# Kernel tuning notes

Hardware: AMD Instinct MI355X
Metric: run time of the kernel (lower is better)

Reference implementation:

```python
import jax, jax.numpy as jnp
import numpy as np

NUM_HEADS = 16
N_EMBD = 1024
HEAD_SIZE = N_EMBD // NUM_HEADS
BLOCK_SIZE = 2048
B, T = 4, 2048


def setup_inputs() -> dict:
    key = jax.random.key(0)
    ks = jax.random.split(key, 6)
    x = jax.random.normal(ks[0], (B, T, N_EMBD), dtype=jnp.float32)
    s = 1.0 / np.sqrt(N_EMBD)
    # per-head q/k/v projections (bias=False), stacked over heads: [H, D, hs]
    Wq = jax.random.uniform(ks[1], (NUM_HEADS, N_EMBD, HEAD_SIZE), minval=-s, maxval=s, dtype=jnp.float32)
    Wk = jax.random.uniform(ks[2], (NUM_HEADS, N_EMBD, HEAD_SIZE), minval=-s, maxval=s, dtype=jnp.float32)
    Wv = jax.random.uniform(ks[3], (NUM_HEADS, N_EMBD, HEAD_SIZE), minval=-s, maxval=s, dtype=jnp.float32)
    # output projection nn.Linear(n_embd, n_embd): weight [D, D] (out, in) + bias [D]
    Wo = jax.random.uniform(ks[4], (N_EMBD, N_EMBD), minval=-s, maxval=s, dtype=jnp.float32)
    bo = jax.random.uniform(ks[5], (N_EMBD,), minval=-s, maxval=s, dtype=jnp.float32)
    return {"x": x, "Wq": Wq, "Wk": Wk, "Wv": Wv, "Wo": Wo, "bo": bo}


def _mha(x, Wq, Wk, Wv, Wo, bo):
    # project all heads at once: [B,T,D] x [H,D,hs] -> [B,H,T,hs]
    q = jnp.einsum("btd,hds->bhts", x, Wq)
    k = jnp.einsum("btd,hds->bhts", x, Wk)
    v = jnp.einsum("btd,hds->bhts", x, Wv)
    scale = jnp.asarray(HEAD_SIZE, x.dtype) ** -0.5
    scores = jnp.einsum("bhqs,bhks->bhqk", q, k) * scale  # [B,H,T,T]
    T_ = x.shape[1]
    causal = jnp.tril(jnp.ones((T_, T_), dtype=bool))
    scores = jnp.where(causal[None, None], scores, jnp.asarray(-jnp.inf, x.dtype))
    att = jax.nn.softmax(scores, axis=-1)
    out = jnp.einsum("bhqk,bhks->bhqs", att, v)  # [B,H,T,hs]
    # concat heads along last dim: [B,T,H*hs]
    out = out.transpose(0, 2, 1, 3).reshape(x.shape[0], T_, N_EMBD)
    # output projection (dropout=0.0 -> identity)
    return out @ Wo.T + bo


def reference(x, Wq, Wk, Wv, Wo, bo):
    return _mha(x, Wq, Wk, Wv, Wo, bo)
```

## Files before the change

### kernel.cpp

```cpp
#include <hip/hip_runtime.h>
#include <hip/hip_bf16.h>
#include <stdint.h>

typedef __bf16 bf16;
typedef __attribute__((ext_vector_type(8))) __bf16 bf16x8;
typedef __attribute__((ext_vector_type(4))) float f32x4;

#define NH     16
#define DM     1024
#define HS     64
#define BATCH  4
#define SEQ    2048
#define N_XE   (BATCH * SEQ * DM)
#define N_WOE  (DM * DM)

__device__ __forceinline__ void async16(void* lds, const void* g) {
  __builtin_amdgcn_global_load_lds(
      (const uint32_t __attribute__((address_space(1)))*)g,
      (uint32_t __attribute__((address_space(3)))*)lds,
      16, 0, 0);
}

__device__ __forceinline__ f32x4 mfma16(bf16x8 a, bf16x8 b, f32x4 c) {
  return __builtin_amdgcn_mfma_f32_16x16x32_bf16(a, b, c, 0, 0, 0);
}

__global__ void detect_mode(const unsigned short* __restrict__ x, int* flag) {
  int lane = threadIdx.x & 63;
  unsigned short v = x[2 * lane];
  int e = (v >> 7) & 0xFF;
  int sane = (e >= 90 && e <= 160) ? 1 : 0;
  #pragma unroll
  for (int s = 1; s < 64; s <<= 1) sane += __shfl_xor(sane, s, 64);
  if (threadIdx.x == 0) *flag = (sane >= 48) ? 0 : 1;
}

__global__ __launch_bounds__(256)
void convert_in(const void* __restrict__ x, const void* __restrict__ Wo,
                bf16* __restrict__ xb, bf16* __restrict__ Wob,
                const int* __restrict__ flagp) {
  const int f32m = *flagp;
  size_t base = ((size_t)blockIdx.x * 256 + threadIdx.x) * 8;
  const void* src; bf16* dst; size_t off;
  if (base < (size_t)N_XE) { src = x;  dst = xb;  off = base; }
  else                     { src = Wo; dst = Wob; off = base - N_XE; }
  if (f32m) {
    const float* s = (const float*)src + off;
    float4 a = *(const float4*)s;
    float4 b = *(const float4*)(s + 4);
    bf16x8 o;
    o[0] = (bf16)a.x; o[1] = (bf16)a.y; o[2] = (bf16)a.z; o[3] = (bf16)a.w;
    o[4] = (bf16)b.x; o[5] = (bf16)b.y; o[6] = (bf16)b.z; o[7] = (bf16)b.w;
    *(bf16x8*)(dst + off) = o;
  } else {
    *(bf16x8*)(dst + off) = *(const bf16x8*)((const bf16*)src + off);
  }
}

__global__ __launch_bounds__(256)
void transpose_w(const void* __restrict__ Wq, const void* __restrict__ Wk,
                 const void* __restrict__ Wv, bf16* __restrict__ WT,
                 const int* __restrict__ flagp) {
  __shared__ bf16 Ts[64][72];
  const int f32m = *flagp;
  const void* W = (blockIdx.y == 0) ? Wq : (blockIdx.y == 1) ? Wk : Wv;
  bf16* dst = WT + (size_t)blockIdx.y * DM * DM;
  const int h  = blockIdx.x >> 4;
  const int d0 = (blockIdx.x & 15) * 64;
  const int tid = threadIdx.x;
  #pragma unroll
  for (int p = 0; p < 2; ++p) {
    int idx = p * 256 + tid;
    int dr = idx >> 3, c = idx & 7;
    size_t eoff = (size_t)(h * DM + d0 + dr) * HS + c * 8;
    bf16x8 v;
    if (f32m) {
      const float* s = (const float*)W + eoff;
      #pragma unroll
      for (int j = 0; j < 8; ++j) v[j] = (bf16)s[j];
    } else {
      v = *(const bf16x8*)((const bf16*)W + eoff);
    }
    #pragma unroll
    for (int j = 0; j < 8; ++j) Ts[c * 8 + j][dr] = v[j];
  }
  __syncthreads();
  #pragma unroll
  for (int p = 0; p < 2; ++p) {
    int idx = p * 256 + tid;
    int sr = idx >> 3, c = idx & 7;
    bf16x8 v = *(const bf16x8*)(&Ts[sr][c * 8]);
    *(bf16x8*)(dst + (size_t)(h * 64 + sr) * DM + d0 + c * 8) = v;
  }
}

template<typename EpiF>
__device__ __forceinline__ void gemm128_bt(const bf16* __restrict__ A,
                                           const bf16* __restrict__ BT,
                                           int m0, int n0, EpiF epi) {
  __shared__ bf16 As[2][128 * 32];
  __shared__ bf16 Bs[2][128 * 32];
  const int tid  = threadIdx.x;
  const int wave = tid >> 6, lane = tid & 63;
  const int wr = wave >> 1, wc = wave & 1;
  const int fr = lane & 15, fg = lane >> 4;
  const int srow = lane >> 2;
  const int scb  = (lane & 3) * 16;
  f32x4 acc[4][4] = {};

  auto STAGE = [&](int buf, int k0) {
    #pragma unroll
    for (int i = 0; i < 2; ++i) {
      int chunk = wave * 2 + i;
      int row = chunk * 16 + srow;
      async16((char*)&As[buf][0] + chunk * 1024,
              (const char*)(A + (size_t)(m0 + row) * DM + k0) + scb);
      async16((char*)&Bs[buf][0] + chunk * 1024,
              (const char*)(BT + (size_t)(n0 + row) * DM + k0) + scb);
    }
  };

  STAGE(0, 0);
  #pragma unroll 1
  for (int t = 0; t < 32; ++t) {
    const int buf = t & 1;
    if (t + 1 < 32) {
      STAGE(buf ^ 1, (t + 1) * 32);
      asm volatile("s_waitcnt vmcnt(4)" ::: "memory");
    } else {
      asm volatile("s_waitcnt vmcnt(0)" ::: "memory");
    }
    __builtin_amdgcn_s_barrier();
    bf16x8 af[4], bv[4];
    #pragma unroll
    for (int mi = 0; mi < 4; ++mi)
      af[mi] = *(const bf16x8*)(&As[buf][(wr * 64 + mi * 16 + fr) * 32 + fg * 8]);
    #pragma unroll
    for (int ni = 0; ni < 4; ++ni)
      bv[ni] = *(const bf16x8*)(&Bs[buf][(wc * 64 + ni * 16 + fr) * 32 + fg * 8]);
    #pragma unroll
    for (int mi = 0; mi < 4; ++mi)
      #pragma unroll
      for (int ni = 0; ni < 4; ++ni)
        acc[mi][ni] = mfma16(af[mi], bv[ni], acc[mi][ni]);
    __builtin_amdgcn_s_barrier();
  }
  #pragma unroll
  for (int mi = 0; mi < 4; ++mi)
    #pragma unroll
    for (int ni = 0; ni < 4; ++ni)
      #pragma unroll
      for (int r = 0; r < 4; ++r) {
        int m = m0 + wr * 64 + mi * 16 + fg * 4 + r;
        int n = n0 + wc * 64 + ni * 16 + fr;
        epi(m, n, acc[mi][ni][r]);
      }
}

__global__ __launch_bounds__(256, 4)
void qkv_gemm(const bf16* __restrict__ x, const bf16* __restrict__ WT,
              bf16* __restrict__ Qb, bf16* __restrict__ Kb, bf16* __restrict__ Vt) {
  const int bid = blockIdx.x;
  const int m0 = (bid & 63) * 128;
  const int nz = bid >> 6;
  const int z  = nz >> 3;
  const int n0 = (nz & 7) * 128;
  const bf16* BT = WT + (size_t)z * DM * DM;
  gemm128_bt(x, BT, m0, n0, [&](int m, int n, float v) {
    int b = m >> 11, t = m & 2047, h = n >> 6, s = n & 63;
    if (z == 0)
      Qb[((size_t)(b * NH + h) * SEQ + t) * HS + s] = (bf16)v;
    else if (z == 1)
      Kb[((size_t)(b * NH + h) * SEQ + t) * HS + s] = (bf16)v;
    else
      Vt[((size_t)(b * NH + h) * HS + s) * SEQ + t] = (bf16)v;
  });
}

__global__ __launch_bounds__(256, 4)
void out_gemm(const bf16* __restrict__ att, const bf16* __restrict__ Wob,
              const void* __restrict__ bo, void* __restrict__ out,
              const int* __restrict__ flagp) {
  const int f32m = *flagp;
  const int bid = blockIdx.x;
  const int m0 = (bid & 63) * 128;
  const int n0 = (bid >> 6) * 128;
  gemm128_bt(att, Wob, m0, n0, [&](int m, int n, float v) {
    float bv = f32m ? ((const float*)bo)[n] : (float)((const bf16*)bo)[n];
    float o = v + bv;
    if (f32m) ((float*)out)[(size_t)m * DM + n] = o;
    else      ((bf16*)out)[(size_t)m * DM + n] = (bf16)o;
  });
}

#define KVB  64
__global__ __launch_bounds__(256, 2)
void attn_kernel(const bf16* __restrict__ Qb, const bf16* __restrict__ Kb,
                 const bf16* __restrict__ Vt, bf16* __restrict__ att) {
  __shared__ bf16 Ks[2][64][64];
  __shared__ bf16 Vs[2][64][64];
  __shared__ bf16 Ps[4][2][16][64];
  const int wave = threadIdx.x >> 6, lane = threadIdx.x & 63;
  const int fr = lane & 15, fg = lane >> 4;
  const int pair = blockIdx.x;
  const int bh = blockIdx.y;
  const bf16* Qp = Qb + (size_t)bh * SEQ * HS;
  const bf16* Kp = Kb + (size_t)bh * SEQ * HS;
  const bf16* Vp = Vt + (size_t)bh * HS * SEQ;
  const int b = bh >> 4, h = bh & 15;

  const int srow8 = lane >> 3;
  const int schk  = (lane & 7) ^ srow8;

  #pragma unroll
  for (int seg = 0; seg < 2; ++seg) {
    const int qb = seg == 0 ? (15 - pair) : pair;
    const int q0 = qb * 128 + wave * 32;
    const int kv_hi = q0 + 32;
    const int nt = (qb + 1) * 2;

    bf16x8 qf[2][2];
    #pragma unroll
    for (int qt = 0; qt < 2; ++qt)
      #pragma unroll
      for (int hh = 0; hh < 2; ++hh)
        qf[qt][hh] = *(const bf16x8*)(Qp + (size_t)(q0 + qt * 16 + fr) * HS + hh * 32 + fg * 8);

    float rs[2][4] = {};
    f32x4 accO[2][4] = {};

    auto STAGE = [&](int buf, int kvb) {
      #pragma unroll
      for (int i = 0; i < 2; ++i) {
        int r8 = wave * 16 + i * 8;
        async16(&Ks[buf][r8][0], Kp + (size_t)(kvb + r8 + srow8) * HS + schk * 8);
        async16(&Vs[buf][r8][0], Vp + (size_t)(r8 + srow8) * SEQ + kvb + schk * 8);
      }
    };

    STAGE(0, 0);
    for (int t = 0; t < nt; ++t) {
      const int buf = t & 1;
      const int kvb = t * KVB;
      if (t + 1 < nt) {
        STAGE(buf ^ 1, kvb + KVB);
        asm volatile("s_waitcnt vmcnt(4)" ::: "memory");
      } else {
        asm volatile("s_waitcnt vmcnt(0)" ::: "memory");
      }
      __builtin_amdgcn_s_barrier();
      if (kvb < kv_hi) {
        bf16x8 kf[4][2];
        #pragma unroll
        for (int s = 0; s < 4; ++s)
          #pragma unroll
          for (int hh = 0; hh < 2; ++hh)
            kf[s][hh] = *(const bf16x8*)(&Ks[buf][s * 16 + fr][((hh * 4 + fg) ^ (fr & 7)) * 8]);
        asm volatile("s_waitcnt lgkmcnt(0)" ::: "memory");

        #pragma unroll
        for (int qt = 0; qt < 2; ++qt) {
          f32x4 sc[4];
          #pragma unroll
          for (int s = 0; s < 4; ++s) {
            sc[s] = f32x4{0.f, 0.f, 0.f, 0.f};
            sc[s] = mfma16(qf[qt][0], kf[s][0], sc[s]);
            sc[s] = mfma16(qf[qt][1], kf[s][1], sc[s]);
          }
          #pragma unroll
          for (int s = 0; s < 4; ++s)
            #pragma unroll
            for (int r = 0; r < 4; ++r) {
              int qrow = q0 + qt * 16 + fg * 4 + r;
              int col  = kvb + s * 16 + fr;
              float p = __expf(sc[s][r] * 0.125f);
              p = (col <= qrow) ? p : 0.f;
              rs[qt][r] += p;
              int row = fg * 4 + r;
              int swz = (s * 2 + (fr >> 3)) ^ (row & 7);
              Ps[wave][qt][row][swz * 8 + (fr & 7)] = (bf16)p;
            }
        }
        asm volatile("s_waitcnt lgkmcnt(0)" ::: "memory");
        __builtin_amdgcn_sched_barrier(0);
        bf16x8 pf[2][2];
        #pragma unroll
        for (int qt = 0; qt < 2; ++qt)
          #pragma unroll
          for (int kc = 0; kc < 2; ++kc)
            pf[qt][kc] = *(const bf16x8*)(&Ps[wave][qt][fr][(((kc * 4 + fg) ^ (fr & 7))) * 8]);
        #pragma unroll
        for (int st = 0; st < 4; ++st) {
          bf16x8 vf0 = *(const bf16x8*)(&Vs[buf][st * 16 + fr][((fg) ^ (fr & 7)) * 8]);
          bf16x8 vf1 = *(const bf16x8*)(&Vs[buf][st * 16 + fr][((4 + fg) ^ (fr & 7)) * 8]);
          #pragma unroll
          for (int qt = 0; qt < 2; ++qt) {
            accO[qt][st] = mfma16(pf[qt][0], vf0, accO[qt][st]);
            accO[qt][st] = mfma16(pf[qt][1], vf1, accO[qt][st]);
          }
        }
      }
      __builtin_amdgcn_s_barrier();
    }

    #pragma unroll
    for (int sh = 1; sh < 16; sh <<= 1)
      #pragma unroll
      for (int qt = 0; qt < 2; ++qt)
        #pragma unroll
        for (int r = 0; r < 4; ++r)
          rs[qt][r] += __shfl_xor(rs[qt][r], sh, 64);
    #pragma unroll
    for (int qt = 0; qt < 2; ++qt)
      #pragma unroll
      for (int st = 0; st < 4; ++st)
        #pragma unroll
        for (int r = 0; r < 4; ++r) {
          int qrow = q0 + qt * 16 + fg * 4 + r;
          float o = accO[qt][st][r] / rs[qt][r];
          att[((size_t)(b * SEQ + qrow)) * DM + h * 64 + st * 16 + fr] = (bf16)o;
        }
  }
}

extern "C" void kernel_launch(void* const* d_in, const int* in_sizes, int n_in,
                              void* d_out, int out_size, void* d_ws, size_t ws_size,
                              hipStream_t stream) {
  const void* x  = d_in[0];
  const void* Wq = d_in[1];
  const void* Wk = d_in[2];
  const void* Wv = d_in[3];
  const void* Wo = d_in[4];
  const void* bo = d_in[5];

  char* ws = (char*)d_ws;
  int*  flag = (int*)ws;
  bf16* xb  = (bf16*)(ws + 256);
  bf16* WT  = (bf16*)(ws + 256 + ((size_t)16 << 20));
  bf16* Wob = (bf16*)(ws + 256 + ((size_t)22 << 20));
  bf16* Qb  = (bf16*)(ws + 256 + ((size_t)24 << 20));
  bf16* Kb  = (bf16*)(ws + 256 + ((size_t)40 << 20));
  bf16* Vt  = (bf16*)(ws + 256 + ((size_t)56 << 20));
  bf16* att = xb;

  detect_mode<<<1, 64, 0, stream>>>((const unsigned short*)x, flag);
  convert_in<<<(N_XE + N_WOE) / 2048, 256, 0, stream>>>(x, Wo, xb, Wob, flag);
  transpose_w<<<dim3(256, 3), 256, 0, stream>>>(Wq, Wk, Wv, WT, flag);
  qkv_gemm<<<dim3(1536), 256, 0, stream>>>(xb, WT, Qb, Kb, Vt);
  attn_kernel<<<dim3(8, BATCH * NH), 256, 0, stream>>>(Qb, Kb, Vt, att);
  out_gemm<<<dim3(512), 256, 0, stream>>>(att, Wob, bo, d_out, flag);
}
```

Baseline: 286.6 us.

## Fuse prep kernels and deepen GEMM k-tile to 64 with swizzled LDS

Merges the dtype detection, input conversion and weight transpose into a single prep launch, with each block probing the input dtype inline instead of through a separate kernel and flag. The shared GEMM now stages 64-wide k-tiles (16 iterations instead of 32), using an XOR-swizzled LDS layout to avoid bank conflicts and s_setprio around the MFMA block. Launch-bound occupancy drops to 2 blocks per CU because of the doubled LDS footprint. The aim is fewer launches and fewer barriers per GEMM, at the cost of lower occupancy and a redundant probe in every block.

```diff
diff --git a/kernel.cpp b/kernel.cpp
--- a/kernel.cpp
+++ b/kernel.cpp
@@ -13,6 +13,7 @@
 #define SEQ    2048
 #define N_XE   (BATCH * SEQ * DM)
 #define N_WOE  (DM * DM)
+#define NCONV  ((N_XE + N_WOE) / 2048)
 
 __device__ __forceinline__ void async16(void* lds, const void* g) {
   __builtin_amdgcn_global_load_lds(
@@ -25,72 +26,73 @@
   return __builtin_amdgcn_mfma_f32_16x16x32_bf16(a, b, c, 0, 0, 0);
 }
 
-__global__ void detect_mode(const unsigned short* __restrict__ x, int* flag) {
+__device__ __forceinline__ int probe_f32(const unsigned short* x) {
   int lane = threadIdx.x & 63;
   unsigned short v = x[2 * lane];
   int e = (v >> 7) & 0xFF;
   int sane = (e >= 90 && e <= 160) ? 1 : 0;
   #pragma unroll
   for (int s = 1; s < 64; s <<= 1) sane += __shfl_xor(sane, s, 64);
-  if (threadIdx.x == 0) *flag = (sane >= 48) ? 0 : 1;
+  return (sane >= 48) ? 0 : 1;
 }
 
 __global__ __launch_bounds__(256)
-void convert_in(const void* __restrict__ x, const void* __restrict__ Wo,
-                bf16* __restrict__ xb, bf16* __restrict__ Wob,
-                const int* __restrict__ flagp) {
-  const int f32m = *flagp;
-  size_t base = ((size_t)blockIdx.x * 256 + threadIdx.x) * 8;
-  const void* src; bf16* dst; size_t off;
-  if (base < (size_t)N_XE) { src = x;  dst = xb;  off = base; }
-  else                     { src = Wo; dst = Wob; off = base - N_XE; }
-  if (f32m) {
-    const float* s = (const float*)src + off;
-    float4 a = *(const float4*)s;
-    float4 b = *(const float4*)(s + 4);
-    bf16x8 o;
-    o[0] = (bf16)a.x; o[1] = (bf16)a.y; o[2] = (bf16)a.z; o[3] = (bf16)a.w;
-    o[4] = (bf16)b.x; o[5] = (bf16)b.y; o[6] = (bf16)b.z; o[7] = (bf16)b.w;
-    *(bf16x8*)(dst + off) = o;
+void prep(const void* __restrict__ x, const void* __restrict__ Wq,
+          const void* __restrict__ Wk, const void* __restrict__ Wv,
+          const void* __restrict__ Wo,
+          bf16* __restrict__ xb, bf16* __restrict__ Wob, bf16* __restrict__ WT) {
+  const int f32m = probe_f32((const unsigned short*)x);
+  const int bid = blockIdx.x;
+  if (bid < NCONV) {
+    size_t base = ((size_t)bid * 256 + threadIdx.x) * 8;
+    const void* src; bf16* dst; size_t off;
+    if (base < (size_t)N_XE) { src = x;  dst = xb;  off = base; }
+    else                     { src = Wo; dst = Wob; off = base - N_XE; }
+    if (f32m) {
+      const float* s = (const float*)src + off;
+      float4 a = *(const float4*)s;
+      float4 b = *(const float4*)(s + 4);
+      bf16x8 o;
+      o[0] = (bf16)a.x; o[1] = (bf16)a.y; o[2] = (bf16)a.z; o[3] = (bf16)a.w;
+      o[4] = (bf16)b.x; o[5] = (bf16)b.y; o[6] = (bf16)b.z; o[7] = (bf16)b.w;
+      *(bf16x8*)(dst + off) = o;
+    } else {
+      *(bf16x8*)(dst + off) = *(const bf16x8*)((const bf16*)src + off);
+    }
   } else {
-    *(bf16x8*)(dst + off) = *(const bf16x8*)((const bf16*)src + off);
-  }
-}
-
-__global__ __launch_bounds__(256)
-void transpose_w(const void* __restrict__ Wq, const void* __restrict__ Wk,
-                 const void* __restrict__ Wv, bf16* __restrict__ WT,
-                 const int* __restrict__ flagp) {
-  __shared__ bf16 Ts[64][72];
-  const int f32m = *flagp;
-  const void* W = (blockIdx.y == 0) ? Wq : (blockIdx.y == 1) ? Wk : Wv;
-  bf16* dst = WT + (size_t)blockIdx.y * DM * DM;
-  const int h  = blockIdx.x >> 4;
-  const int d0 = (blockIdx.x & 15) * 64;
-  const int tid = threadIdx.x;
-  #pragma unroll
-  for (int p = 0; p < 2; ++p) {
-    int idx = p * 256 + tid;
-    int dr = idx >> 3, c = idx & 7;
-    size_t eoff = (size_t)(h * DM + d0 + dr) * HS + c * 8;
-    bf16x8 v;
-    if (f32m) {
-      const float* s = (const float*)W + eoff;
-      #pragma unroll
-      for (int j = 0; j < 8; ++j) v[j] = (bf16)s[j];
-    } else {
-      v = *(const bf16x8*)((const bf16*)W + eoff);
-    }
-    #pragma unroll
-    for (int j = 0; j < 8; ++j) Ts[c * 8 + j][dr] = v[j];
-  }
-  __syncthreads();
-  #pragma unroll
-  for (int p = 0; p < 2; ++p) {
-    int idx = p * 256 + tid;
-    int sr = idx >> 3, c = idx & 7;
-    bf16x8 v = *(const bf16x8*)(&Ts[sr][c * 8]);
-    *(bf16x8*)(dst + (size_t)(h * 64 + sr) * DM + d0 + c * 8) = v;
+    __shared__ bf16 Ts[64][72];
+    const int tb = bid - NCONV;
+    const int wz = tb >> 8;
+    const int tx = tb & 255;
+    const void* W = (wz == 0) ? Wq : (wz == 1) ? Wk : Wv;
+    bf16* dst = WT + (size_t)wz * DM * DM;
+    const int h  = tx >> 4;
+    const int d0 = (tx & 15) * 64;
+    const int tid = threadIdx.x;
+    #pragma unroll
+    for (int p = 0; p < 2; ++p) {
+      int idx = p * 256 + tid;
+      int dr = idx >> 3, c = idx & 7;
+      size_t eoff = (size_t)(h * DM + d0 + dr) * HS + c * 8;
+      bf16x8 v;
+      if (f32m) {
+        const float* s = (const float*)W + eoff;
+        #pragma unroll
+        for (int j = 0; j < 8; ++j) v[j] = (bf16)s[j];
+      } else {
+        v = *(const bf16x8*)((const bf16*)W + eoff);
+      }
+      #pragma unroll
+      for (int j = 0; j < 8; ++j) Ts[c * 8 + j][dr] = v[j];
+    }
+    __syncthreads();
+    #pragma unroll
+    for (int p = 0; p < 2; ++p) {
+      int idx = p * 256 + tid;
+      int sr = idx >> 3, c = idx & 7;
+      bf16x8 v = *(const bf16x8*)(&Ts[sr][c * 8]);
+      *(bf16x8*)(dst + (size_t)(h * 64 + sr) * DM + d0 + c * 8) = v;
+    }
   }
 }
 
@@ -98,51 +100,63 @@
 __device__ __forceinline__ void gemm128_bt(const bf16* __restrict__ A,
                                            const bf16* __restrict__ BT,
                                            int m0, int n0, EpiF epi) {
-  __shared__ bf16 As[2][128 * 32];
-  __shared__ bf16 Bs[2][128 * 32];
+  __shared__ bf16 As[2][128 * 64];
+  __shared__ bf16 Bs[2][128 * 64];
   const int tid  = threadIdx.x;
   const int wave = tid >> 6, lane = tid & 63;
   const int wr = wave >> 1, wc = wave & 1;
   const int fr = lane & 15, fg = lane >> 4;
-  const int srow = lane >> 2;
-  const int scb  = (lane & 3) * 16;
+  const int srow8 = lane >> 3;
+  const int schk  = (lane & 7) ^ srow8;
   f32x4 acc[4][4] = {};
 
-  auto STAGE = [&](int buf, int k0) {
-    #pragma unroll
-    for (int i = 0; i < 2; ++i) {
-      int chunk = wave * 2 + i;
-      int row = chunk * 16 + srow;
-      async16((char*)&As[buf][0] + chunk * 1024,
-              (const char*)(A + (size_t)(m0 + row) * DM + k0) + scb);
-      async16((char*)&Bs[buf][0] + chunk * 1024,
-              (const char*)(BT + (size_t)(n0 + row) * DM + k0) + scb);
+  auto STAGE = [&](int buf, int kt) {
+    const int k0 = kt * 64;
+    #pragma unroll
+    for (int i = 0; i < 4; ++i) {
+      int r8 = wave * 32 + i * 8;
+      async16((char*)&As[buf][0] + (wave * 4 + i) * 1024,
+              A + (size_t)(m0 + r8 + srow8) * DM + k0 + schk * 8);
+      async16((char*)&Bs[buf][0] + (wave * 4 + i) * 1024,
+              BT + (size_t)(n0 + r8 + srow8) * DM + k0 + schk * 8);
     }
   };
 
   STAGE(0, 0);
   #pragma unroll 1
-  for (int t = 0; t < 32; ++t) {
-    const int buf = t & 1;
-    if (t + 1 < 32) {
-      STAGE(buf ^ 1, (t + 1) * 32);
-      asm volatile("s_waitcnt vmcnt(4)" ::: "memory");
+  for (int kt = 0; kt < 16; ++kt) {
+    const int buf = kt & 1;
+    if (kt + 1 < 16) {
+      STAGE(buf ^ 1, kt + 1);
+      asm volatile("s_waitcnt vmcnt(8)" ::: "memory");
     } else {
       asm volatile("s_waitcnt vmcnt(0)" ::: "memory");
     }
     __builtin_amdgcn_s_barrier();
-    bf16x8 af[4], bv[4];
+    bf16x8 af[4][2], bv[4][2];
+    #pragma unroll
+    for (int mi = 0; mi < 4; ++mi) {
+      int r = wr * 64 + mi * 16 + fr;
+      #pragma unroll
+      for (int kk = 0; kk < 2; ++kk)
+        af[mi][kk] = *(const bf16x8*)(&As[buf][r * 64 + (((kk * 4 + fg) ^ (r & 7)) * 8)]);
+    }
+    #pragma unroll
+    for (int ni = 0; ni < 4; ++ni) {
+      int r = wc * 64 + ni * 16 + fr;
+      #pragma unroll
+      for (int kk = 0; kk < 2; ++kk)
+        bv[ni][kk] = *(const bf16x8*)(&Bs[buf][r * 64 + (((kk * 4 + fg) ^ (r & 7)) * 8)]);
+    }
+    __builtin_amdgcn_s_setprio(1);
     #pragma unroll
     for (int mi = 0; mi < 4; ++mi)
-      af[mi] = *(const bf16x8*)(&As[buf][(wr * 64 + mi * 16 + fr) * 32 + fg * 8]);
-    #pragma unroll
-    for (int ni = 0; ni < 4; ++ni)
-      bv[ni] = *(const bf16x8*)(&Bs[buf][(wc * 64 + ni * 16 + fr) * 32 + fg * 8]);
-    #pragma unroll
-    for (int mi = 0; mi < 4; ++mi)
       #pragma unroll
       for (int ni = 0; ni < 4; ++ni)
-        acc[mi][ni] = mfma16(af[mi], bv[ni], acc[mi][ni]);
+        #pragma unroll
+        for (int kk = 0; kk < 2; ++kk)
+          acc[mi][ni] = mfma16(af[mi][kk], bv[ni][kk], acc[mi][ni]);
+    __builtin_amdgcn_s_setprio(0);
     __builtin_amdgcn_s_barrier();
   }
   #pragma unroll
@@ -157,7 +171,7 @@
       }
 }
 
-__global__ __launch_bounds__(256, 4)
+__global__ __launch_bounds__(256, 2)
 void qkv_gemm(const bf16* __restrict__ x, const bf16* __restrict__ WT,
               bf16* __restrict__ Qb, bf16* __restrict__ Kb, bf16* __restrict__ Vt) {
   const int bid = blockIdx.x;
@@ -177,11 +191,11 @@
   });
 }
 
-__global__ __launch_bounds__(256, 4)
+__global__ __launch_bounds__(256, 2)
 void out_gemm(const bf16* __restrict__ att, const bf16* __restrict__ Wob,
               const void* __restrict__ bo, void* __restrict__ out,
-              const int* __restrict__ flagp) {
-  const int f32m = *flagp;
+              const unsigned short* __restrict__ xprobe) {
+  const int f32m = probe_f32(xprobe);
   const int bid = blockIdx.x;
   const int m0 = (bid & 63) * 128;
   const int n0 = (bid >> 6) * 128;
@@ -334,19 +348,17 @@
   const void* bo = d_in[5];
 
   char* ws = (char*)d_ws;
-  int*  flag = (int*)ws;
-  bf16* xb  = (bf16*)(ws + 256);
-  bf16* WT  = (bf16*)(ws + 256 + ((size_t)16 << 20));
-  bf16* Wob = (bf16*)(ws + 256 + ((size_t)22 << 20));
-  bf16* Qb  = (bf16*)(ws + 256 + ((size_t)24 << 20));
-  bf16* Kb  = (bf16*)(ws + 256 + ((size_t)40 << 20));
-  bf16* Vt  = (bf16*)(ws + 256 + ((size_t)56 << 20));
+  bf16* xb  = (bf16*)(ws);
+  bf16* WT  = (bf16*)(ws + ((size_t)16 << 20));
+  bf16* Wob = (bf16*)(ws + ((size_t)22 << 20));
+  bf16* Qb  = (bf16*)(ws + ((size_t)24 << 20));
+  bf16* Kb  = (bf16*)(ws + ((size_t)40 << 20));
+  bf16* Vt  = (bf16*)(ws + ((size_t)56 << 20));
   bf16* att = xb;
 
-  detect_mode<<<1, 64, 0, stream>>>((const unsigned short*)x, flag);
-  convert_in<<<(N_XE + N_WOE) / 2048, 256, 0, stream>>>(x, Wo, xb, Wob, flag);
-  transpose_w<<<dim3(256, 3), 256, 0, stream>>>(Wq, Wk, Wv, WT, flag);
+  prep<<<dim3(NCONV + 768), 256, 0, stream>>>(x, Wq, Wk, Wv, Wo, xb, Wob, WT);
   qkv_gemm<<<dim3(1536), 256, 0, stream>>>(xb, WT, Qb, Kb, Vt);
   attn_kernel<<<dim3(8, BATCH * NH), 256, 0, stream>>>(Qb, Kb, Vt, att);
-  out_gemm<<<dim3(512), 256, 0, stream>>>(att, Wob, bo, d_out, flag);
-}
+  out_gemm<<<dim3(512), 256, 0, stream>>>(att, Wob, bo, d_out,
+                                          (const unsigned short*)x);
+}
```

Result: faster. 276.0 us (-3.7%).
